# Performance work log

Measured on AMD Instinct MI355X. Metric: run time of the kernel, lower is better.

The kernel has to match this reference:

```python
import jax, jax.numpy as jnp
import numpy as np
import math

SIZE = 64
NLAND = 8
N_ITER = 6


def setup_inputs() -> dict:
    key = jax.random.key(0)
    k1, k2, k3 = jax.random.split(key, 3)
    B, T, C = 4, 4096, 1024
    return {
        "q": jax.random.normal(k1, (B, T, C), dtype=jnp.float32),
        "k": jax.random.normal(k2, (B, T, C), dtype=jnp.float32),
        "v": jax.random.normal(k3, (B, T, C), dtype=jnp.float32),
    }


def _iterative_pinv(mat, n_iter=N_ITER):
    # Newton-Schulz iteration for pseudo-inverse of [..., m, m] kernel.
    m = mat.shape[-1]
    I = jnp.eye(m, dtype=mat.dtype)
    K = mat
    # NOTE: torch.max over the whole tensor (global scalar), faithful to source.
    V = (1.0 / jnp.max(jnp.sum(K, axis=-2))) * jnp.swapaxes(K, -1, -2)
    for _ in range(n_iter):
        KV = jnp.matmul(K, V)
        V = jnp.matmul(0.25 * V, 13.0 * I - jnp.matmul(KV, 15.0 * I - jnp.matmul(KV, 7.0 * I - KV)))
    return V


def reference(q, k, v):
    B, T, C = q.shape
    H = C // SIZE
    scale = 1.0 / math.sqrt(SIZE)
    # Faithful reshape (not transpose) as in the source module.
    qh = q.reshape(B, H, T, SIZE)
    kh = k.reshape(B, H, T, SIZE)
    vh = v.reshape(B, H, T, SIZE)
    # T % NLAND == 0 branch: landmark = segment mean over T//NLAND tokens.
    q_l = qh.reshape(B, H, NLAND, T // NLAND, SIZE).mean(axis=-2)  # [B,H,m,d]
    k_l = kh.reshape(B, H, NLAND, T // NLAND, SIZE).mean(axis=-2)
    kernel_1 = jax.nn.softmax(jnp.einsum('bhtd,bhmd->bhtm', qh, k_l) * scale, axis=-1)  # [B,H,T,m]
    kernel_2 = jax.nn.softmax(jnp.einsum('bhmd,bhnd->bhmn', q_l, k_l) * scale, axis=-1)  # [B,H,m,m]
    kernel_3 = jax.nn.softmax(jnp.einsum('bhmd,bhtd->bhmt', q_l, kh) * scale, axis=-1)  # [B,H,m,T]
    pinv = _iterative_pinv(kernel_2)  # [B,H,m,m]
    k3v = jnp.matmul(kernel_3, vh)    # [B,H,m,d]
    out = jnp.matmul(jnp.matmul(kernel_1, pinv), k3v)  # [B,H,T,d]
    return out.reshape(B, T, C)
```

## Files before the change

kernel.cpp:

```cpp
#include <hip/hip_runtime.h>
#include <math.h>

#define T_TOK 4096
#define DD 64
#define NHEADS 64
#define SEG 512
#define SCALE 0.125f

#define QL_OFF   0
#define KL_OFF   32768
#define K2_OFF   65536
#define CS_OFF   69632
#define KP_OFF   70144
#define PA_OFF   332288
#define PD_OFF   2429440
#define W2_OFF   2462208

#define WAVE_BAR() __builtin_amdgcn_wave_barrier()

__global__ __launch_bounds__(256) void qsum_kernel(
    const float* __restrict__ q, float* __restrict__ ws) {
  int tid = threadIdx.x;
  const float4* q4 = (const float4*)q + (size_t)blockIdx.x * 8192;
  float4 b[2][8];
#pragma unroll
  for (int i = 0; i < 8; ++i) b[0][i] = q4[i * 256 + tid];
  float4 a = make_float4(0.f, 0.f, 0.f, 0.f);
#pragma unroll
  for (int j = 0; j < 4; ++j) {
    if (j < 3) {
#pragma unroll
      for (int i = 0; i < 8; ++i)
        b[(j + 1) & 1][i] = q4[(j + 1) * 2048 + i * 256 + tid];
    }
#pragma unroll
    for (int i = 0; i < 8; ++i) {
      float4 x = b[j & 1][i];
      a.x += x.x; a.y += x.y; a.z += x.z; a.w += x.w;
    }
  }
  __shared__ float4 red[16][17];
  red[tid >> 4][tid & 15] = a;
  __syncthreads();
  if (tid < 16) {
    float4 s = make_float4(0.f, 0.f, 0.f, 0.f);
#pragma unroll
    for (int g = 0; g < 16; ++g) {
      float4 r = red[g][tid];
      s.x += r.x; s.y += r.y; s.z += r.z; s.w += r.w;
    }
    const float inv = 1.f / (float)SEG;
    s.x *= inv; s.y *= inv; s.z *= inv; s.w *= inv;
    ((float4*)(ws + QL_OFF))[blockIdx.x * 16 + tid] = s;
  }
}

__global__ __launch_bounds__(256) void kvpass_kernel(
    const float* __restrict__ k, const float* __restrict__ v,
    float* __restrict__ ws) {
  int tid = threadIdx.x;
  int w = tid >> 6, lane = tid & 63;
  int gw = blockIdx.x * 4 + w;
  int hb = gw >> 6;
  __shared__ float qls[8][68];
  __shared__ float kt_all[4][16][68];
  __shared__ float vt_all[4][16][68];
  __shared__ float pl_all[4][16][9];
  float (*kt)[68] = kt_all[w];
  float (*vt)[68] = vt_all[w];
  float (*pl)[9]  = pl_all[w];

  if (tid < 128) {
    float4 x = ((const float4*)(ws + QL_OFF))[hb * 128 + tid];
    *(float4*)&qls[tid >> 4][(tid & 15) * 4] = x;
  }
  __syncthreads();

  int m = lane & 7, g = lane >> 4, d4i = lane & 15;
  size_t tokbase = (size_t)gw * 64;
  const float4* k4 = (const float4*)k + tokbase * 16;
  const float4* v4 = (const float4*)v + tokbase * 16;

  float4 ks = make_float4(0.f, 0.f, 0.f, 0.f);
  float den = 0.f;
  float4 acc0 = make_float4(0.f, 0.f, 0.f, 0.f);
  float4 acc1 = make_float4(0.f, 0.f, 0.f, 0.f);

#pragma unroll 1
  for (int tile = 0; tile < 4; ++tile) {
    float4 k0 = k4[tile * 256 + lane];
    float4 k1 = k4[tile * 256 + 64 + lane];
    float4 k2 = k4[tile * 256 + 128 + lane];
    float4 k3 = k4[tile * 256 + 192 + lane];
    float4 v0 = v4[tile * 256 + lane];
    float4 v1 = v4[tile * 256 + 64 + lane];
    float4 v2 = v4[tile * 256 + 128 + lane];
    float4 v3 = v4[tile * 256 + 192 + lane];
    int r0 = lane >> 4, c0 = (lane & 15) * 4;
    *(float4*)&kt[r0][c0] = k0;      *(float4*)&vt[r0][c0] = v0;
    *(float4*)&kt[r0 + 4][c0] = k1;  *(float4*)&vt[r0 + 4][c0] = v1;
    *(float4*)&kt[r0 + 8][c0] = k2;  *(float4*)&vt[r0 + 8][c0] = v2;
    *(float4*)&kt[r0 + 12][c0] = k3; *(float4*)&vt[r0 + 12][c0] = v3;
    ks.x += k0.x + k1.x + k2.x + k3.x;
    ks.y += k0.y + k1.y + k2.y + k3.y;
    ks.z += k0.z + k1.z + k2.z + k3.z;
    ks.w += k0.w + k1.w + k2.w + k3.w;
    WAVE_BAR();
#pragma unroll
    for (int rep = 0; rep < 2; ++rep) {
      int t = rep * 8 + (lane >> 3);
      const float4* kr = (const float4*)&kt[t][0];
      const float4* qr = (const float4*)&qls[m][0];
      float dp = 0.f;
#pragma unroll
      for (int d4 = 0; d4 < 16; ++d4) {
        float4 kv = kr[d4], qv = qr[d4];
        dp += kv.x * qv.x + kv.y * qv.y + kv.z * qv.z + kv.w * qv.w;
      }
      float p = __expf(dp * SCALE);
      pl[t][m] = p;
      den += p;
    }
    WAVE_BAR();
#pragma unroll
    for (int t = 0; t < 16; ++t) {
      float4 vv = *(const float4*)&vt[t][d4i * 4];
      float pa = pl[t][g];
      float pb = pl[t][g + 4];
      acc0.x += pa * vv.x; acc0.y += pa * vv.y; acc0.z += pa * vv.z; acc0.w += pa * vv.w;
      acc1.x += pb * vv.x; acc1.y += pb * vv.y; acc1.z += pb * vv.z; acc1.w += pb * vv.w;
    }
    WAVE_BAR();
  }
  ks.x += __shfl_xor(ks.x, 16, 64); ks.y += __shfl_xor(ks.y, 16, 64);
  ks.z += __shfl_xor(ks.z, 16, 64); ks.w += __shfl_xor(ks.w, 16, 64);
  ks.x += __shfl_xor(ks.x, 32, 64); ks.y += __shfl_xor(ks.y, 32, 64);
  ks.z += __shfl_xor(ks.z, 32, 64); ks.w += __shfl_xor(ks.w, 32, 64);
  if (lane < 16)
    ((float4*)(ws + KP_OFF))[gw * 16 + lane] = ks;
  den += __shfl_xor(den, 8, 64);
  den += __shfl_xor(den, 16, 64);
  den += __shfl_xor(den, 32, 64);
  if (lane < 8)
    ws[PD_OFF + (size_t)gw * 8 + lane] = den;
  ((float4*)(ws + PA_OFF))[((size_t)gw * 8 + g) * 16 + d4i] = acc0;
  ((float4*)(ws + PA_OFF))[((size_t)gw * 8 + g + 4) * 16 + d4i] = acc1;
}

__global__ __launch_bounds__(512) void prepk_kernel(float* __restrict__ ws) {
  int hb = blockIdx.x, tid = threadIdx.x;
  __shared__ float qls[8][68];
  __shared__ float kls[8][68];
  __shared__ float ee[8][9];
  int m = tid >> 6, d = tid & 63;
  float s = 0.f;
#pragma unroll
  for (int j = 0; j < 8; ++j)
    s += ws[KP_OFF + (size_t)(hb * 64 + m * 8 + j) * 64 + d];
  s *= (1.f / (float)SEG);
  kls[m][d] = s;
  ws[KL_OFF + hb * 512 + tid] = s;
  qls[m][d] = ws[QL_OFF + hb * 512 + tid];
  __syncthreads();
  if (tid < 64) {
    int i = tid >> 3, j = tid & 7;
    float dot = 0.f;
#pragma unroll
    for (int dd = 0; dd < 64; ++dd) dot += qls[i][dd] * kls[j][dd];
    ee[i][j] = __expf(dot * SCALE);
  }
  __syncthreads();
  if (tid < 64) {
    int i = tid >> 3, j = tid & 7;
    float ssum = 0.f;
#pragma unroll
    for (int jj = 0; jj < 8; ++jj) ssum += ee[i][jj];
    ws[K2_OFF + hb * 64 + tid] = ee[i][j] / ssum;
  }
  if (tid < 8) {
    float cs = 0.f;
    for (int ii = 0; ii < 8; ++ii) {
      float ssum = 0.f;
#pragma unroll
      for (int jj = 0; jj < 8; ++jj) ssum += ee[ii][jj];
      cs += ee[ii][tid] / ssum;
    }
    ws[CS_OFF + hb * 8 + tid] = cs;
  }
}

__global__ __launch_bounds__(512) void pinvw2_kernel(float* __restrict__ ws) {
  int hb = blockIdx.x, tid = threadIdx.x;
  __shared__ float k3vs[8][68];
  __shared__ float K[8][9], V[8][9], X[8][9], Y[8][9];
  __shared__ float smax;
  int m = tid >> 6, d = tid & 63;
  float s = 0.f, den = 0.f;
  for (int c = 0; c < 64; ++c) {
    s += ws[PA_OFF + (((size_t)hb * 64 + c) * 8 + m) * 64 + d];
    den += ws[PD_OFF + ((size_t)hb * 64 + c) * 8 + m];
  }
  k3vs[m][d] = s / den;
  if (tid < 64) {
    float mx = 0.f;
    for (int t = 0; t < 8; ++t) mx = fmaxf(mx, ws[CS_OFF + t * 64 + tid]);
    for (int off = 32; off; off >>= 1) mx = fmaxf(mx, __shfl_xor(mx, off, 64));
    if (tid == 0) smax = mx;
  }
  int i = (tid >> 3) & 7, j = tid & 7;
  if (tid < 64) K[i][j] = ws[K2_OFF + hb * 64 + tid];
  __syncthreads();
  if (tid < 64) V[i][j] = K[j][i] * (1.f / smax);
  __syncthreads();
  for (int it = 0; it < 6; ++it) {
    float x = 0.f;
    if (tid < 64) {
      for (int kk = 0; kk < 8; ++kk) x += K[i][kk] * V[kk][j];
      X[i][j] = x;
    }
    __syncthreads();
    float bm = 0.f;
    if (tid < 64) {
      for (int kk = 0; kk < 8; ++kk) bm += X[i][kk] * X[kk][j];
      bm = 7.f * x - bm;
      Y[i][j] = bm;
    }
    __syncthreads();
    float dm = 0.f;
    if (tid < 64) {
      for (int kk = 0; kk < 8; ++kk) dm += X[i][kk] * Y[kk][j];
      dm = 15.f * x - dm;
    }
    __syncthreads();
    if (tid < 64) Y[i][j] = dm;
    __syncthreads();
    float vd = 0.f;
    if (tid < 64) {
      for (int kk = 0; kk < 8; ++kk) vd += V[i][kk] * Y[kk][j];
      vd = 0.25f * (13.f * V[i][j] - vd);
    }
    __syncthreads();
    if (tid < 64) V[i][j] = vd;
    __syncthreads();
  }
  float o = 0.f;
#pragma unroll
  for (int jj = 0; jj < 8; ++jj) o += V[m][jj] * k3vs[jj][d];
  ws[W2_OFF + hb * 512 + tid] = o;
}

__global__ __launch_bounds__(256) void out_kernel(
    const float* __restrict__ q, float* __restrict__ out,
    const float* __restrict__ ws) {
  int tid = threadIdx.x;
  int w = tid >> 6, lane = tid & 63;
  int gw = blockIdx.x * 4 + w;
  int hb = gw >> 6;
  __shared__ float qt_all[4][16][68];
  __shared__ float pl_all[4][16][9];
  __shared__ float w2_all[4][8][68];
  float (*qt)[68] = qt_all[w];
  float (*pl)[9]  = pl_all[w];
  float (*w2)[68] = w2_all[w];

  int m = lane & 7;
  float4 klrow[16];
#pragma unroll
  for (int d4 = 0; d4 < 16; ++d4)
    klrow[d4] = ((const float4*)(ws + KL_OFF))[hb * 128 + m * 16 + d4];
#pragma unroll
  for (int i = 0; i < 2; ++i) {
    int f4 = i * 64 + lane;
    float4 y = ((const float4*)(ws + W2_OFF))[hb * 128 + f4];
    *(float4*)&w2[f4 >> 4][(f4 & 15) * 4] = y;
  }

  size_t base4 = (size_t)gw * 1024;
  const float4* q4 = (const float4*)q + base4;
  float4* o4 = (float4*)out + base4;
  float4 buf[2][4];
#pragma unroll
  for (int i = 0; i < 4; ++i) buf[0][i] = q4[i * 64 + lane];

#pragma unroll
  for (int tile = 0; tile < 4; ++tile) {
    int cur = tile & 1;
    if (tile < 3) {
#pragma unroll
      for (int i = 0; i < 4; ++i)
        buf[cur ^ 1][i] = q4[(tile + 1) * 256 + i * 64 + lane];
    }
#pragma unroll
    for (int i = 0; i < 4; ++i) {
      int f4 = i * 64 + lane;
      *(float4*)&qt[f4 >> 4][(f4 & 15) * 4] = buf[cur][i];
    }
    WAVE_BAR();
#pragma unroll
    for (int rep = 0; rep < 2; ++rep) {
      int t = rep * 8 + (lane >> 3);
      const float4* qr = (const float4*)&qt[t][0];
      float dot = 0.f;
#pragma unroll
      for (int d4 = 0; d4 < 16; ++d4) {
        float4 a = qr[d4];
        dot += a.x * klrow[d4].x + a.y * klrow[d4].y +
               a.z * klrow[d4].z + a.w * klrow[d4].w;
      }
      pl[t][m] = __expf(dot * SCALE);
    }
    WAVE_BAR();
#pragma unroll
    for (int i = 0; i < 4; ++i) {
      int t = i * 4 + (lane >> 4);
      int qd = lane & 15;
      float p0 = pl[t][0], p1 = pl[t][1], p2 = pl[t][2], p3 = pl[t][3];
      float p4 = pl[t][4], p5 = pl[t][5], p6 = pl[t][6], p7 = pl[t][7];
      float inv = 1.f / (p0 + p1 + p2 + p3 + p4 + p5 + p6 + p7);
      float4 acc = make_float4(0.f, 0.f, 0.f, 0.f);
      float pm[8] = {p0, p1, p2, p3, p4, p5, p6, p7};
#pragma unroll
      for (int m2 = 0; m2 < 8; ++m2) {
        float wgt = pm[m2] * inv;
        float4 wv = *(const float4*)&w2[m2][qd * 4];
        acc.x += wgt * wv.x; acc.y += wgt * wv.y;
        acc.z += wgt * wv.z; acc.w += wgt * wv.w;
      }
      o4[tile * 256 + i * 64 + lane] = acc;
    }
    WAVE_BAR();
  }
}

extern "C" void kernel_launch(void* const* d_in, const int* in_sizes, int n_in,
                              void* d_out, int out_size, void* d_ws, size_t ws_size,
                              hipStream_t stream) {
  const float* q = (const float*)d_in[0];
  const float* k = (const float*)d_in[1];
  const float* v = (const float*)d_in[2];
  float* out = (float*)d_out;
  float* ws = (float*)d_ws;

  qsum_kernel<<<512, 256, 0, stream>>>(q, ws);
  kvpass_kernel<<<1024, 256, 0, stream>>>(k, v, ws);
  prepk_kernel<<<NHEADS, 512, 0, stream>>>(ws);
  pinvw2_kernel<<<NHEADS, 512, 0, stream>>>(ws);
  out_kernel<<<1024, 256, 0, stream>>>(q, out, ws);
}
```

Measured before the change: 83.15 us.

## Split q-sum into more blocks and double-buffer k/v loads in kvpass

After: 87.02 us. 1.05x slower.

```diff
diff --git a/kernel.cpp b/kernel.cpp
--- a/kernel.cpp
+++ b/kernel.cpp
@@ -15,29 +15,21 @@
 #define PA_OFF   332288
 #define PD_OFF   2429440
 #define W2_OFF   2462208
+#define LPQ_OFF  2494976
 
 #define WAVE_BAR() __builtin_amdgcn_wave_barrier()
 
 __global__ __launch_bounds__(256) void qsum_kernel(
     const float* __restrict__ q, float* __restrict__ ws) {
   int tid = threadIdx.x;
-  const float4* q4 = (const float4*)q + (size_t)blockIdx.x * 8192;
-  float4 b[2][8];
-#pragma unroll
-  for (int i = 0; i < 8; ++i) b[0][i] = q4[i * 256 + tid];
+  const float4* q4 = (const float4*)q + (size_t)blockIdx.x * 2048;
+  float4 x[8];
+#pragma unroll
+  for (int i = 0; i < 8; ++i) x[i] = q4[i * 256 + tid];
   float4 a = make_float4(0.f, 0.f, 0.f, 0.f);
 #pragma unroll
-  for (int j = 0; j < 4; ++j) {
-    if (j < 3) {
-#pragma unroll
-      for (int i = 0; i < 8; ++i)
-        b[(j + 1) & 1][i] = q4[(j + 1) * 2048 + i * 256 + tid];
-    }
-#pragma unroll
-    for (int i = 0; i < 8; ++i) {
-      float4 x = b[j & 1][i];
-      a.x += x.x; a.y += x.y; a.z += x.z; a.w += x.w;
-    }
+  for (int i = 0; i < 8; ++i) {
+    a.x += x[i].x; a.y += x[i].y; a.z += x[i].z; a.w += x[i].w;
   }
   __shared__ float4 red[16][17];
   red[tid >> 4][tid & 15] = a;
@@ -49,11 +41,56 @@
       float4 r = red[g][tid];
       s.x += r.x; s.y += r.y; s.z += r.z; s.w += r.w;
     }
-    const float inv = 1.f / (float)SEG;
-    s.x *= inv; s.y *= inv; s.z *= inv; s.w *= inv;
-    ((float4*)(ws + QL_OFF))[blockIdx.x * 16 + tid] = s;
-  }
-}
+    ((float4*)(ws + LPQ_OFF))[blockIdx.x * 16 + tid] = s;
+  }
+}
+
+__global__ __launch_bounds__(512) void prepq_kernel(float* __restrict__ ws) {
+  int hb = blockIdx.x, tid = threadIdx.x;
+  int m = tid >> 6, d = tid & 63;
+  float s = 0.f;
+#pragma unroll
+  for (int c2 = 0; c2 < 4; ++c2)
+    s += ws[LPQ_OFF + (size_t)(hb * 32 + m * 4 + c2) * 64 + d];
+  ws[QL_OFF + hb * 512 + tid] = s * (1.f / (float)SEG);
+}
+
+#define STAGE_AND_CONSUME(K0,K1,K2,K3,V0,V1,V2,V3)                            \
+  {                                                                           \
+    int r0_ = lane >> 4, c0_ = (lane & 15) * 4;                               \
+    *(float4*)&kt[r0_][c0_] = K0;       *(float4*)&vt[r0_][c0_] = V0;         \
+    *(float4*)&kt[r0_+4][c0_] = K1;     *(float4*)&vt[r0_+4][c0_] = V1;       \
+    *(float4*)&kt[r0_+8][c0_] = K2;     *(float4*)&vt[r0_+8][c0_] = V2;       \
+    *(float4*)&kt[r0_+12][c0_] = K3;    *(float4*)&vt[r0_+12][c0_] = V3;      \
+    ks.x += K0.x+K1.x+K2.x+K3.x; ks.y += K0.y+K1.y+K2.y+K3.y;                 \
+    ks.z += K0.z+K1.z+K2.z+K3.z; ks.w += K0.w+K1.w+K2.w+K3.w;                 \
+  }                                                                           \
+  WAVE_BAR();                                                                 \
+  _Pragma("unroll")                                                           \
+  for (int rep_ = 0; rep_ < 2; ++rep_) {                                      \
+    int t_ = rep_ * 8 + (lane >> 3);                                          \
+    const float4* kr_ = (const float4*)&kt[t_][0];                            \
+    const float4* qr_ = (const float4*)&qls[m][0];                            \
+    float dp_ = 0.f;                                                          \
+    _Pragma("unroll")                                                         \
+    for (int d4_ = 0; d4_ < 16; ++d4_) {                                      \
+      float4 kv_ = kr_[d4_], qv_ = qr_[d4_];                                  \
+      dp_ += kv_.x*qv_.x + kv_.y*qv_.y + kv_.z*qv_.z + kv_.w*qv_.w;           \
+    }                                                                         \
+    float p_ = __expf(dp_ * SCALE);                                           \
+    pl[t_][m] = p_;                                                           \
+    den += p_;                                                                \
+  }                                                                           \
+  WAVE_BAR();                                                                 \
+  _Pragma("unroll")                                                           \
+  for (int t_ = 0; t_ < 16; ++t_) {                                           \
+    float4 vv_ = *(const float4*)&vt[t_][d4i * 4];                            \
+    float pa_ = pl[t_][g];                                                    \
+    float pb_ = pl[t_][g + 4];                                                \
+    acc0.x += pa_*vv_.x; acc0.y += pa_*vv_.y; acc0.z += pa_*vv_.z; acc0.w += pa_*vv_.w; \
+    acc1.x += pb_*vv_.x; acc1.y += pb_*vv_.y; acc1.z += pb_*vv_.z; acc1.w += pb_*vv_.w; \
+  }                                                                           \
+  WAVE_BAR();
 
 __global__ __launch_bounds__(256) void kvpass_kernel(
     const float* __restrict__ k, const float* __restrict__ v,
@@ -86,51 +123,29 @@
   float4 acc0 = make_float4(0.f, 0.f, 0.f, 0.f);
   float4 acc1 = make_float4(0.f, 0.f, 0.f, 0.f);
 
+  float4 ka0 = k4[lane],       ka1 = k4[64 + lane],
+         ka2 = k4[128 + lane], ka3 = k4[192 + lane];
+  float4 va0 = v4[lane],       va1 = v4[64 + lane],
+         va2 = v4[128 + lane], va3 = v4[192 + lane];
+
 #pragma unroll 1
-  for (int tile = 0; tile < 4; ++tile) {
-    float4 k0 = k4[tile * 256 + lane];
-    float4 k1 = k4[tile * 256 + 64 + lane];
-    float4 k2 = k4[tile * 256 + 128 + lane];
-    float4 k3 = k4[tile * 256 + 192 + lane];
-    float4 v0 = v4[tile * 256 + lane];
-    float4 v1 = v4[tile * 256 + 64 + lane];
-    float4 v2 = v4[tile * 256 + 128 + lane];
-    float4 v3 = v4[tile * 256 + 192 + lane];
-    int r0 = lane >> 4, c0 = (lane & 15) * 4;
-    *(float4*)&kt[r0][c0] = k0;      *(float4*)&vt[r0][c0] = v0;
-    *(float4*)&kt[r0 + 4][c0] = k1;  *(float4*)&vt[r0 + 4][c0] = v1;
-    *(float4*)&kt[r0 + 8][c0] = k2;  *(float4*)&vt[r0 + 8][c0] = v2;
-    *(float4*)&kt[r0 + 12][c0] = k3; *(float4*)&vt[r0 + 12][c0] = v3;
-    ks.x += k0.x + k1.x + k2.x + k3.x;
-    ks.y += k0.y + k1.y + k2.y + k3.y;
-    ks.z += k0.z + k1.z + k2.z + k3.z;
-    ks.w += k0.w + k1.w + k2.w + k3.w;
-    WAVE_BAR();
-#pragma unroll
-    for (int rep = 0; rep < 2; ++rep) {
-      int t = rep * 8 + (lane >> 3);
-      const float4* kr = (const float4*)&kt[t][0];
-      const float4* qr = (const float4*)&qls[m][0];
-      float dp = 0.f;
-#pragma unroll
-      for (int d4 = 0; d4 < 16; ++d4) {
-        float4 kv = kr[d4], qv = qr[d4];
-        dp += kv.x * qv.x + kv.y * qv.y + kv.z * qv.z + kv.w * qv.w;
-      }
-      float p = __expf(dp * SCALE);
-      pl[t][m] = p;
-      den += p;
-    }
-    WAVE_BAR();
-#pragma unroll
-    for (int t = 0; t < 16; ++t) {
-      float4 vv = *(const float4*)&vt[t][d4i * 4];
-      float pa = pl[t][g];
-      float pb = pl[t][g + 4];
-      acc0.x += pa * vv.x; acc0.y += pa * vv.y; acc0.z += pa * vv.z; acc0.w += pa * vv.w;
-      acc1.x += pb * vv.x; acc1.y += pb * vv.y; acc1.z += pb * vv.z; acc1.w += pb * vv.w;
-    }
-    WAVE_BAR();
+  for (int t2 = 0; t2 < 2; ++t2) {
+    int bB = (t2 * 2 + 1) * 256;
+    float4 kb0 = k4[bB + lane],       kb1 = k4[bB + 64 + lane],
+           kb2 = k4[bB + 128 + lane], kb3 = k4[bB + 192 + lane];
+    float4 vb0 = v4[bB + lane],       vb1 = v4[bB + 64 + lane],
+           vb2 = v4[bB + 128 + lane], vb3 = v4[bB + 192 + lane];
+
+    STAGE_AND_CONSUME(ka0, ka1, ka2, ka3, va0, va1, va2, va3)
+
+    if (t2 == 0) {
+      ka0 = k4[512 + lane];       ka1 = k4[512 + 64 + lane];
+      ka2 = k4[512 + 128 + lane]; ka3 = k4[512 + 192 + lane];
+      va0 = v4[512 + lane];       va1 = v4[512 + 64 + lane];
+      va2 = v4[512 + 128 + lane]; va3 = v4[512 + 192 + lane];
+    }
+
+    STAGE_AND_CONSUME(kb0, kb1, kb2, kb3, vb0, vb1, vb2, vb3)
   }
   ks.x += __shfl_xor(ks.x, 16, 64); ks.y += __shfl_xor(ks.y, 16, 64);
   ks.z += __shfl_xor(ks.z, 16, 64); ks.w += __shfl_xor(ks.w, 16, 64);
@@ -341,7 +356,8 @@
   float* out = (float*)d_out;
   float* ws = (float*)d_ws;
 
-  qsum_kernel<<<512, 256, 0, stream>>>(q, ws);
+  qsum_kernel<<<2048, 256, 0, stream>>>(q, ws);
+  prepq_kernel<<<NHEADS, 512, 0, stream>>>(ws);
   kvpass_kernel<<<1024, 256, 0, stream>>>(k, v, ws);
   prepk_kernel<<<NHEADS, 512, 0, stream>>>(ws);
   pinvw2_kernel<<<NHEADS, 512, 0, stream>>>(ws);
```
